# Kernel optimization log

Measured on AMD Instinct MI355X. Metric: run time of the kernel, lower is better.

The kernel has to match this reference:

```python
import jax, jax.numpy as jnp
import numpy as np

NUM_CLASSES = 1000
EMBED_DIM = 256
N = 131072
MOMENTUM = 0.995
EPS = 1e-12  # F.normalize default eps


def _l2norm(x):
    # F.normalize: x / max(||x||_2, eps)
    n = jnp.sqrt(jnp.sum(x * x, axis=-1, keepdims=True))
    return x / jnp.maximum(n, EPS)


def setup_inputs() -> dict:
    key = jax.random.key(0)
    k1, k2, k3, k4 = jax.random.split(key, 4)
    z = jax.random.normal(k1, (N, EMBED_DIM), dtype=jnp.float32)
    prototypes = _l2norm(jax.random.normal(k2, (NUM_CLASSES, EMBED_DIM), dtype=jnp.float32))
    initialized = jax.random.randint(k3, (NUM_CLASSES,), 0, 2) > 0
    labels = jax.random.randint(k4, (N,), 0, NUM_CLASSES)
    return {"z": z, "prototypes": prototypes, "initialized": initialized, "labels": labels}


def reference(z, prototypes, initialized, labels):
    # Fused segment-mean-by-label + EMA-normalize update (ema_update).
    sums = jax.ops.segment_sum(z, labels, num_segments=NUM_CLASSES)          # [C, D]
    counts = jax.ops.segment_sum(jnp.ones((z.shape[0],), z.dtype), labels,
                                 num_segments=NUM_CLASSES)                    # [C]
    present = counts > 0                                                      # [C]
    mean_z = sums / jnp.maximum(counts, 1.0)[:, None]                         # [C, D]
    mean_n = _l2norm(mean_z)
    ema = _l2norm(MOMENTUM * prototypes + (1.0 - MOMENTUM) * mean_n)
    cand = jnp.where(initialized[:, None], ema, mean_n)
    new_protos = jnp.where(present[:, None], cand, prototypes)
    return new_protos
```

## Files before the change

kernel.cpp:

```cpp
#include <hip/hip_runtime.h>
#include <math.h>

static constexpr int   kC    = 1000;
static constexpr int   kD    = 256;
static constexpr int   kCap  = 1024;
static constexpr int   kCntS = 16;
static constexpr float kMom  = 0.995f;
static constexpr float kEps  = 1e-12f;

typedef float f32x4 __attribute__((ext_vector_type(4)));

__device__ __forceinline__ f32x4 nt_load4(const float* p) {
    return __builtin_nontemporal_load((const f32x4*)p);
}

__device__ __forceinline__ float block_sum256(float v) {
    __shared__ float lds[4];
    #pragma unroll
    for (int off = 32; off > 0; off >>= 1) v += __shfl_down(v, off, 64);
    __syncthreads();
    if ((threadIdx.x & 63) == 0) lds[threadIdx.x >> 6] = v;
    __syncthreads();
    return lds[0] + lds[1] + lds[2] + lds[3];
}

__global__ void k_scatter(const int* __restrict__ labels, int n,
                          int* __restrict__ cnt ,
                          int* __restrict__ idx,
                          int* __restrict__ ovf ) {
    const int t = blockIdx.x * 256 + threadIdx.x;
    const int i0 = t * 4;
    if (i0 >= n) return;
    if (i0 + 3 < n) {
        const int4 l4 = ((const int4*)labels)[t];
        #pragma unroll
        for (int k = 0; k < 4; ++k) {
            const int lab = (&l4.x)[k];
            const int i = i0 + k;
            const int p = atomicAdd(&cnt[lab * kCntS], 1);
            if (p < kCap) {
                idx[(size_t)lab * kCap + p] = i;
            } else {
                const int q = atomicAdd(&ovf[0], 1);
                ovf[1 + 2 * q] = lab; ovf[2 + 2 * q] = i;
            }
        }
    } else {
        for (int i = i0; i < n; ++i) {
            const int lab = labels[i];
            const int p = atomicAdd(&cnt[lab * kCntS], 1);
            if (p < kCap) {
                idx[(size_t)lab * kCap + p] = i;
            } else {
                const int q = atomicAdd(&ovf[0], 1);
                ovf[1 + 2 * q] = lab; ovf[2 + 2 * q] = i;
            }
        }
    }
}

__global__ void __launch_bounds__(256, 4)
k_reduce(const float* __restrict__ z, const float* __restrict__ protos,
         const int* __restrict__ initialized, const int* __restrict__ cnt,
         const int* __restrict__ idx, const int* __restrict__ ovf,
         float* __restrict__ out) {
    __shared__ int   sh_idx[kCap];
    __shared__ float sh_part[4][kD];

    const int c    = blockIdx.x;
    const int tid  = threadIdx.x;
    const int wave = tid >> 6;
    const int lane = tid & 63;

    const int cntc = cnt[c * kCntS];
    const int m    = min(cntc, kCap);
    const int* __restrict__ cidx = idx + (size_t)c * kCap;

    for (int j = tid; j < m; j += 256) sh_idx[j] = cidx[j];
    __syncthreads();

    f32x4 acc0 = {0.f, 0.f, 0.f, 0.f};
    f32x4 acc1 = {0.f, 0.f, 0.f, 0.f};

    int r = wave;
    for (; r + 28 < m; r += 32) {
        const int i0 = sh_idx[r +  0]; const int i1 = sh_idx[r +  4];
        const int i2 = sh_idx[r +  8]; const int i3 = sh_idx[r + 12];
        const int i4 = sh_idx[r + 16]; const int i5 = sh_idx[r + 20];
        const int i6 = sh_idx[r + 24]; const int i7 = sh_idx[r + 28];
        const f32x4 a0 = nt_load4(z + (size_t)i0 * kD + lane * 4);
        const f32x4 a1 = nt_load4(z + (size_t)i1 * kD + lane * 4);
        const f32x4 a2 = nt_load4(z + (size_t)i2 * kD + lane * 4);
        const f32x4 a3 = nt_load4(z + (size_t)i3 * kD + lane * 4);
        const f32x4 a4 = nt_load4(z + (size_t)i4 * kD + lane * 4);
        const f32x4 a5 = nt_load4(z + (size_t)i5 * kD + lane * 4);
        const f32x4 a6 = nt_load4(z + (size_t)i6 * kD + lane * 4);
        const f32x4 a7 = nt_load4(z + (size_t)i7 * kD + lane * 4);
        acc0 += a0 + a1;
        acc1 += a2 + a3;
        acc0 += a4 + a5;
        acc1 += a6 + a7;
    }
    for (; r < m; r += 4) {
        acc0 += nt_load4(z + (size_t)sh_idx[r] * kD + lane * 4);
    }
    acc0 += acc1;

    ((f32x4*)&sh_part[wave][lane * 4])[0] = acc0;
    __syncthreads();

    const int d = tid;
    float sum = sh_part[0][d] + sh_part[1][d] + sh_part[2][d] + sh_part[3][d];

    const int novf = ovf[0];
    if (novf > 0) {
        for (int j = 0; j < novf; ++j) {
            if (ovf[1 + 2 * j] == c) sum += z[(size_t)ovf[2 + 2 * j] * kD + d];
        }
    }

    const float mean   = sum / fmaxf((float)cntc, 1.0f);
    const float nrm    = sqrtf(block_sum256(mean * mean));
    const float mean_n = mean / fmaxf(nrm, kEps);

    const float p    = protos[c * kD + d];
    const float e    = kMom * p + (1.0f - kMom) * mean_n;
    const float nrm2 = sqrtf(block_sum256(e * e));
    const float ema  = e / fmaxf(nrm2, kEps);

    const float cand = (initialized[c] != 0) ? ema : mean_n;
    __builtin_nontemporal_store((cntc > 0) ? cand : p, &out[c * kD + d]);
}

__global__ void k_atomic_accum(const float* __restrict__ z,
                               const int* __restrict__ labels, int n,
                               float* __restrict__ sums, int* __restrict__ counts) {
    const int i = blockIdx.x;
    const int d = threadIdx.x;
    if (i >= n) return;
    const int lab = labels[i];
    atomicAdd(&sums[lab * kD + d], z[i * kD + d]);
    if (d == 0) atomicAdd(&counts[lab], 1);
}

__global__ void k_finalize_from_sums(const float* __restrict__ protos,
                                     const int* __restrict__ initialized,
                                     const int* __restrict__ counts,
                                     float* __restrict__ out) {
    const int c = blockIdx.x;
    const int d = threadIdx.x;
    const int cntc = counts[c];
    const float sum = out[c * kD + d];

    const float mean   = sum / fmaxf((float)cntc, 1.0f);
    const float nrm    = sqrtf(block_sum256(mean * mean));
    const float mean_n = mean / fmaxf(nrm, kEps);

    const float p    = protos[c * kD + d];
    const float e    = kMom * p + (1.0f - kMom) * mean_n;
    const float nrm2 = sqrtf(block_sum256(e * e));
    const float ema  = e / fmaxf(nrm2, kEps);

    const float cand = (initialized[c] != 0) ? ema : mean_n;
    out[c * kD + d] = (cntc > 0) ? cand : p;
}

extern "C" void kernel_launch(void* const* d_in, const int* in_sizes, int n_in,
                              void* d_out, int out_size, void* d_ws, size_t ws_size,
                              hipStream_t stream) {
    const float* z           = (const float*)d_in[0];
    const float* protos      = (const float*)d_in[1];
    const int*   initialized = (const int*)d_in[2];
    const int*   labels      = (const int*)d_in[3];
    const int n = in_sizes[3];
    float* out = (float*)d_out;

    int* ws  = (int*)d_ws;
    int* cnt = ws;
    int* ovf = ws + 1024 * kCntS;
    int* idx = ws + 1024 * kCntS + 8 + 2 * n;
    const size_t need = (size_t)(1024 * kCntS + 8 + 2 * (size_t)n
                                 + (size_t)kC * kCap) * sizeof(int);

    if (ws_size >= need) {
        (void)hipMemsetAsync(ws, 0, (size_t)(1024 * kCntS + 8) * sizeof(int),
                             stream);
        const int threads = (n + 3) / 4;
        const int blocks = (threads + 255) / 256;
        k_scatter<<<blocks, 256, 0, stream>>>(labels, n, cnt, idx, ovf);
        k_reduce <<<kC, kD, 0, stream>>>(z, protos, initialized, cnt, idx,
                                         ovf, out);
    } else {
        int* counts = ws;
        (void)hipMemsetAsync(counts, 0, kC * sizeof(int), stream);
        (void)hipMemsetAsync(out, 0, (size_t)kC * kD * sizeof(float), stream);
        k_atomic_accum<<<n, kD, 0, stream>>>(z, labels, n, out, counts);
        k_finalize_from_sums<<<kC, kD, 0, stream>>>(protos, initialized, counts, out);
    }
}
```

Baseline: 43.42 us.

## Replace global-atomic label bucketing with per-stripe LDS histograms and prefix scan

Adds a new two-kernel path. Each block bins one 1024-label stripe using shared-memory atomics and writes a per-stripe count matrix plus per-stripe index buckets. The reduce kernel then prefix-scans each class's counts across stripes and gathers the indices before the same z accumulation and normalization. This removes the workspace memset and the contended global atomics. In exchange it needs a very large workspace, and the count and index reads in the reduce are strided and uncoalesced. The old atomic-accumulate fallback is removed, and the old path remains only when the new workspace does not fit.

Result: faster. 37.60 us (-13.4%).

```diff
diff --git a/kernel.cpp b/kernel.cpp
--- a/kernel.cpp
+++ b/kernel.cpp
@@ -1,12 +1,13 @@
 #include <hip/hip_runtime.h>
 #include <math.h>
 
-static constexpr int   kC    = 1000;
-static constexpr int   kD    = 256;
-static constexpr int   kCap  = 1024;
-static constexpr int   kCntS = 16;
-static constexpr float kMom  = 0.995f;
-static constexpr float kEps  = 1e-12f;
+static constexpr int   kC      = 1000;
+static constexpr int   kStripe = 1024;
+static constexpr int   kD      = 256;
+static constexpr int   kCap    = 1024;
+static constexpr int   kCntS   = 16;
+static constexpr float kMom    = 0.995f;
+static constexpr float kEps    = 1e-12f;
 
 typedef float f32x4 __attribute__((ext_vector_type(4)));
 
@@ -24,37 +25,146 @@
     return lds[0] + lds[1] + lds[2] + lds[3];
 }
 
+__global__ void __launch_bounds__(256)
+k_scatter2(const int* __restrict__ labels, int n,
+           unsigned short* __restrict__ cntmat,
+           int* __restrict__ idx) {
+    __shared__ unsigned int hcnt[kC];
+    const int b   = blockIdx.x;
+    const int tid = threadIdx.x;
+
+    for (int c = tid; c < kC; c += 256) hcnt[c] = 0;
+    __syncthreads();
+
+    const int base = b * kStripe;
+    const int m = min(kStripe, n - base);
+    const size_t sbase = (size_t)b * kC * kStripe;
+
+    if (m == kStripe) {
+        const int4 l4 = ((const int4*)(labels + base))[tid];
+        #pragma unroll
+        for (int k = 0; k < 4; ++k) {
+            const int lab = (&l4.x)[k];
+            const unsigned int p = atomicAdd(&hcnt[lab], 1u);
+            idx[sbase + (size_t)lab * kStripe + p] = base + tid * 4 + k;
+        }
+    } else {
+        for (int j = tid; j < m; j += 256) {
+            const int lab = labels[base + j];
+            const unsigned int p = atomicAdd(&hcnt[lab], 1u);
+            idx[sbase + (size_t)lab * kStripe + p] = base + j;
+        }
+    }
+    __syncthreads();
+    for (int c = tid; c < kC; c += 256)
+        cntmat[(size_t)b * kC + c] = (unsigned short)hcnt[c];
+}
+
+__global__ void __launch_bounds__(256, 4)
+k_reduce2(const float* __restrict__ z, const float* __restrict__ protos,
+          const int* __restrict__ initialized,
+          const unsigned short* __restrict__ cntmat, int B,
+          const int* __restrict__ idx, float* __restrict__ out) {
+    __shared__ int          sh_idx[kStripe];
+    __shared__ float        sh_part[4][kD];
+    __shared__ unsigned int s_pfx[256];
+
+    const int c    = blockIdx.x;
+    const int tid  = threadIdx.x;
+    const int wave = tid >> 6;
+    const int lane = tid & 63;
+
+    const unsigned int myc = (tid < B) ? cntmat[(size_t)tid * kC + c] : 0u;
+
+    s_pfx[tid] = myc;
+    __syncthreads();
+    for (int off = 1; off < 256; off <<= 1) {
+        const unsigned int add = (tid >= off) ? s_pfx[tid - off] : 0u;
+        __syncthreads();
+        s_pfx[tid] += add;
+        __syncthreads();
+    }
+    const unsigned int T  = s_pfx[255];
+    const unsigned int ex = s_pfx[tid] - myc;
+
+    f32x4 acc0 = {0.f, 0.f, 0.f, 0.f};
+    f32x4 acc1 = {0.f, 0.f, 0.f, 0.f};
+
+    for (unsigned int cb = 0; cb < T; cb += kStripe) {
+        __syncthreads();
+        if (myc > 0) {
+            const size_t sb = ((size_t)tid * kC + c) * kStripe;
+            for (unsigned int q = 0; q < myc; ++q) {
+                const unsigned int g = ex + q;
+                if (g >= cb && g < cb + kStripe) sh_idx[g - cb] = idx[sb + q];
+            }
+        }
+        __syncthreads();
+
+        const int mm = (int)min((unsigned int)kStripe, T - cb);
+        int r = wave;
+        for (; r + 28 < mm; r += 32) {
+            const int i0 = sh_idx[r +  0]; const int i1 = sh_idx[r +  4];
+            const int i2 = sh_idx[r +  8]; const int i3 = sh_idx[r + 12];
+            const int i4 = sh_idx[r + 16]; const int i5 = sh_idx[r + 20];
+            const int i6 = sh_idx[r + 24]; const int i7 = sh_idx[r + 28];
+            const f32x4 a0 = nt_load4(z + (size_t)i0 * kD + lane * 4);
+            const f32x4 a1 = nt_load4(z + (size_t)i1 * kD + lane * 4);
+            const f32x4 a2 = nt_load4(z + (size_t)i2 * kD + lane * 4);
+            const f32x4 a3 = nt_load4(z + (size_t)i3 * kD + lane * 4);
+            const f32x4 a4 = nt_load4(z + (size_t)i4 * kD + lane * 4);
+            const f32x4 a5 = nt_load4(z + (size_t)i5 * kD + lane * 4);
+            const f32x4 a6 = nt_load4(z + (size_t)i6 * kD + lane * 4);
+            const f32x4 a7 = nt_load4(z + (size_t)i7 * kD + lane * 4);
+            acc0 += a0 + a1;
+            acc1 += a2 + a3;
+            acc0 += a4 + a5;
+            acc1 += a6 + a7;
+        }
+        for (; r < mm; r += 4) {
+            acc0 += nt_load4(z + (size_t)sh_idx[r] * kD + lane * 4);
+        }
+    }
+    acc0 += acc1;
+
+    __syncthreads();
+    ((f32x4*)&sh_part[wave][lane * 4])[0] = acc0;
+    __syncthreads();
+
+    const int d = tid;
+    const float sum = sh_part[0][d] + sh_part[1][d] + sh_part[2][d] + sh_part[3][d];
+    const int cntc = (int)T;
+
+    const float mean   = sum / fmaxf((float)cntc, 1.0f);
+    const float nrm    = sqrtf(block_sum256(mean * mean));
+    const float mean_n = mean / fmaxf(nrm, kEps);
+
+    const float p    = protos[c * kD + d];
+    const float e    = kMom * p + (1.0f - kMom) * mean_n;
+    const float nrm2 = sqrtf(block_sum256(e * e));
+    const float ema  = e / fmaxf(nrm2, kEps);
+
+    const float cand = (initialized[c] != 0) ? ema : mean_n;
+    __builtin_nontemporal_store((cntc > 0) ? cand : p, &out[c * kD + d]);
+}
+
 __global__ void k_scatter(const int* __restrict__ labels, int n,
                           int* __restrict__ cnt ,
                           int* __restrict__ idx,
-                          int* __restrict__ ovf ) {
+                          int* __restrict__ ovf) {
     const int t = blockIdx.x * 256 + threadIdx.x;
     const int i0 = t * 4;
     if (i0 >= n) return;
-    if (i0 + 3 < n) {
-        const int4 l4 = ((const int4*)labels)[t];
-        #pragma unroll
-        for (int k = 0; k < 4; ++k) {
-            const int lab = (&l4.x)[k];
-            const int i = i0 + k;
-            const int p = atomicAdd(&cnt[lab * kCntS], 1);
-            if (p < kCap) {
-                idx[(size_t)lab * kCap + p] = i;
-            } else {
-                const int q = atomicAdd(&ovf[0], 1);
-                ovf[1 + 2 * q] = lab; ovf[2 + 2 * q] = i;
-            }
-        }
-    } else {
-        for (int i = i0; i < n; ++i) {
-            const int lab = labels[i];
-            const int p = atomicAdd(&cnt[lab * kCntS], 1);
-            if (p < kCap) {
-                idx[(size_t)lab * kCap + p] = i;
-            } else {
-                const int q = atomicAdd(&ovf[0], 1);
-                ovf[1 + 2 * q] = lab; ovf[2 + 2 * q] = i;
-            }
+    const int lim = min(4, n - i0);
+    for (int k = 0; k < lim; ++k) {
+        const int i = i0 + k;
+        const int lab = labels[i];
+        const int p = atomicAdd(&cnt[lab * kCntS], 1);
+        if (p < kCap) {
+            idx[(size_t)lab * kCap + p] = i;
+        } else {
+            const int q = atomicAdd(&ovf[0], 1);
+            ovf[1 + 2 * q] = lab; ovf[2 + 2 * q] = i;
         }
     }
 }
@@ -81,7 +191,6 @@
 
     f32x4 acc0 = {0.f, 0.f, 0.f, 0.f};
     f32x4 acc1 = {0.f, 0.f, 0.f, 0.f};
-
     int r = wave;
     for (; r + 28 < m; r += 32) {
         const int i0 = sh_idx[r +  0]; const int i1 = sh_idx[r +  4];
@@ -96,14 +205,10 @@
         const f32x4 a5 = nt_load4(z + (size_t)i5 * kD + lane * 4);
         const f32x4 a6 = nt_load4(z + (size_t)i6 * kD + lane * 4);
         const f32x4 a7 = nt_load4(z + (size_t)i7 * kD + lane * 4);
-        acc0 += a0 + a1;
-        acc1 += a2 + a3;
-        acc0 += a4 + a5;
-        acc1 += a6 + a7;
-    }
-    for (; r < m; r += 4) {
-        acc0 += nt_load4(z + (size_t)sh_idx[r] * kD + lane * 4);
-    }
+        acc0 += a0 + a1; acc1 += a2 + a3;
+        acc0 += a4 + a5; acc1 += a6 + a7;
+    }
+    for (; r < m; r += 4) acc0 += nt_load4(z + (size_t)sh_idx[r] * kD + lane * 4);
     acc0 += acc1;
 
     ((f32x4*)&sh_part[wave][lane * 4])[0] = acc0;
@@ -111,58 +216,21 @@
 
     const int d = tid;
     float sum = sh_part[0][d] + sh_part[1][d] + sh_part[2][d] + sh_part[3][d];
-
     const int novf = ovf[0];
     if (novf > 0) {
-        for (int j = 0; j < novf; ++j) {
+        for (int j = 0; j < novf; ++j)
             if (ovf[1 + 2 * j] == c) sum += z[(size_t)ovf[2 + 2 * j] * kD + d];
-        }
     }
 
     const float mean   = sum / fmaxf((float)cntc, 1.0f);
     const float nrm    = sqrtf(block_sum256(mean * mean));
     const float mean_n = mean / fmaxf(nrm, kEps);
-
     const float p    = protos[c * kD + d];
     const float e    = kMom * p + (1.0f - kMom) * mean_n;
     const float nrm2 = sqrtf(block_sum256(e * e));
     const float ema  = e / fmaxf(nrm2, kEps);
-
     const float cand = (initialized[c] != 0) ? ema : mean_n;
     __builtin_nontemporal_store((cntc > 0) ? cand : p, &out[c * kD + d]);
-}
-
-__global__ void k_atomic_accum(const float* __restrict__ z,
-                               const int* __restrict__ labels, int n,
-                               float* __restrict__ sums, int* __restrict__ counts) {
-    const int i = blockIdx.x;
-    const int d = threadIdx.x;
-    if (i >= n) return;
-    const int lab = labels[i];
-    atomicAdd(&sums[lab * kD + d], z[i * kD + d]);
-    if (d == 0) atomicAdd(&counts[lab], 1);
-}
-
-__global__ void k_finalize_from_sums(const float* __restrict__ protos,
-                                     const int* __restrict__ initialized,
-                                     const int* __restrict__ counts,
-                                     float* __restrict__ out) {
-    const int c = blockIdx.x;
-    const int d = threadIdx.x;
-    const int cntc = counts[c];
-    const float sum = out[c * kD + d];
-
-    const float mean   = sum / fmaxf((float)cntc, 1.0f);
-    const float nrm    = sqrtf(block_sum256(mean * mean));
-    const float mean_n = mean / fmaxf(nrm, kEps);
-
-    const float p    = protos[c * kD + d];
-    const float e    = kMom * p + (1.0f - kMom) * mean_n;
-    const float nrm2 = sqrtf(block_sum256(e * e));
-    const float ema  = e / fmaxf(nrm2, kEps);
-
-    const float cand = (initialized[c] != 0) ? ema : mean_n;
-    out[c * kD + d] = (cntc > 0) ? cand : p;
 }
 
 extern "C" void kernel_launch(void* const* d_in, const int* in_sizes, int n_in,
@@ -175,26 +243,26 @@
     const int n = in_sizes[3];
     float* out = (float*)d_out;
 
+    const int B = (n + kStripe - 1) / kStripe;
+    const size_t cnt_bytes = (((size_t)B * kC * sizeof(unsigned short)) + 255) & ~(size_t)255;
+    const size_t need2 = cnt_bytes + (size_t)B * kC * kStripe * sizeof(int);
+
+    if (B <= 256 && ws_size >= need2) {
+        unsigned short* cntmat = (unsigned short*)d_ws;
+        int* idx = (int*)((char*)d_ws + cnt_bytes);
+        k_scatter2<<<B, 256, 0, stream>>>(labels, n, cntmat, idx);
+        k_reduce2 <<<kC, 256, 0, stream>>>(z, protos, initialized, cntmat, B,
+                                           idx, out);
+        return;
+    }
+
     int* ws  = (int*)d_ws;
     int* cnt = ws;
     int* ovf = ws + 1024 * kCntS;
     int* idx = ws + 1024 * kCntS + 8 + 2 * n;
-    const size_t need = (size_t)(1024 * kCntS + 8 + 2 * (size_t)n
-                                 + (size_t)kC * kCap) * sizeof(int);
-
-    if (ws_size >= need) {
-        (void)hipMemsetAsync(ws, 0, (size_t)(1024 * kCntS + 8) * sizeof(int),
-                             stream);
-        const int threads = (n + 3) / 4;
-        const int blocks = (threads + 255) / 256;
-        k_scatter<<<blocks, 256, 0, stream>>>(labels, n, cnt, idx, ovf);
-        k_reduce <<<kC, kD, 0, stream>>>(z, protos, initialized, cnt, idx,
-                                         ovf, out);
-    } else {
-        int* counts = ws;
-        (void)hipMemsetAsync(counts, 0, kC * sizeof(int), stream);
-        (void)hipMemsetAsync(out, 0, (size_t)kC * kD * sizeof(float), stream);
-        k_atomic_accum<<<n, kD, 0, stream>>>(z, labels, n, out, counts);
-        k_finalize_from_sums<<<kC, kD, 0, stream>>>(protos, initialized, counts, out);
-    }
-}
+    (void)hipMemsetAsync(ws, 0, (size_t)(1024 * kCntS + 8) * sizeof(int), stream);
+    const int threads = (n + 3) / 4;
+    const int blocks = (threads + 255) / 256;
+    k_scatter<<<blocks, 256, 0, stream>>>(labels, n, cnt, idx, ovf);
+    k_reduce <<<kC, 256, 0, stream>>>(z, protos, initialized, cnt, idx, ovf, out);
+}
```
